# Optimization experiments

Measured on AMD Instinct MI355X. Metric: run time of the kernel, lower is better.

## Reference

```python
import jax, jax.numpy as jnp
import numpy as np
import math

B, S, HID = 2, 1024, 2048
N_HEAD, N_KV = 16, 4
HEAD = HID // N_HEAD          # 128
N_REP = N_HEAD // N_KV        # 4


def setup_inputs() -> dict:
    key = jax.random.key(0)
    ks = jax.random.split(key, 5)
    x = jax.random.normal(ks[0], (B, S, HID), dtype=jnp.float32)
    # realistic RoPE tables: freqs over half dim, duplicated (rotate_half convention)
    inv_freq = 1.0 / (10000.0 ** (np.arange(0, HEAD, 2, dtype=np.float32) / HEAD))
    t = np.arange(S, dtype=np.float32)
    freqs = np.outer(t, inv_freq)                    # [S, HEAD/2]
    emb = np.concatenate([freqs, freqs], axis=-1)    # [S, HEAD]
    cos = jnp.asarray(np.cos(emb), dtype=jnp.float32)
    sin = jnp.asarray(np.sin(emb), dtype=jnp.float32)
    sc = 0.02
    wq = jax.random.normal(ks[1], (HID, HID), dtype=jnp.float32) * sc
    wk = jax.random.normal(ks[2], (HID, N_KV * HEAD), dtype=jnp.float32) * sc
    wv = jax.random.normal(ks[3], (HID, N_KV * HEAD), dtype=jnp.float32) * sc
    wo = jax.random.normal(ks[4], (HID, HID), dtype=jnp.float32) * sc
    return {"x": x, "cos": cos, "sin": sin, "wq": wq, "wk": wk, "wv": wv, "wo": wo}


def _rotate_half(t):
    h = t.shape[-1] // 2
    return jnp.concatenate([-t[..., h:], t[..., :h]], axis=-1)


def reference(x, cos, sin, wq, wk, wv, wo):
    b, s, _ = x.shape
    q = (x @ wq).reshape(b, s, N_HEAD, HEAD)   # [B,S,H,D]
    k = (x @ wk).reshape(b, s, N_KV, HEAD)     # [B,S,Kv,D]
    v = (x @ wv).reshape(b, s, N_KV, HEAD)
    # RoPE: cos/sin [S,D] -> [S,1,D], broadcasts over batch and heads
    c = cos[:s, None, :]
    sn = sin[:s, None, :]
    q = q * c + _rotate_half(q) * sn
    k = k * c + _rotate_half(k) * sn
    # GQA: repeat kv heads to match query heads
    k = jnp.repeat(k, N_REP, axis=2)           # [B,S,H,D]
    v = jnp.repeat(v, N_REP, axis=2)
    q = q.transpose(0, 2, 1, 3)                # [B,H,S,D]
    k = k.transpose(0, 2, 1, 3)
    v = v.transpose(0, 2, 1, 3)
    scores = jnp.einsum("bhqd,bhkd->bhqk", q, k) / math.sqrt(HEAD)
    causal = jnp.triu(jnp.full((s, s), -jnp.inf, dtype=scores.dtype), k=1)
    scores = scores + causal[None, None, :, :]
    probs = jax.nn.softmax(scores.astype(jnp.float32), axis=-1).astype(q.dtype)
    out = jnp.einsum("bhqk,bhkd->bhqd", probs, v)   # [B,H,S,D]
    out = out.transpose(0, 2, 1, 3).reshape(b, s, N_HEAD * HEAD)
    return out @ wo
```

## Files before the change

### kernel.cpp

```cpp
#include <hip/hip_runtime.h>
#include <hip/hip_bf16.h>
#include <math.h>
#include <stdint.h>

#define BATCH 2
#define SEQ   1024
#define HID   2048
#define NH    16
#define NKV   4
#define HEAD  128
#define MROWS (BATCH*SEQ)
#define QSC   0.08838834764831845f

typedef _Float16 f16;
typedef _Float16 f16x8 __attribute__((ext_vector_type(8)));
typedef __fp16   h16x2 __attribute__((ext_vector_type(2)));
typedef float    f32x4 __attribute__((ext_vector_type(4)));

__device__ __forceinline__ void glds16(const void* g, void* l) {
    __builtin_amdgcn_global_load_lds(
        (const __attribute__((address_space(1))) void*)g,
        (__attribute__((address_space(3))) void*)l, 16, 0, 0);
}

__device__ __forceinline__ f32x4 mfma16(f16x8 a, f16x8 b, f32x4 c) {
    return __builtin_amdgcn_mfma_f32_16x16x32_f16(a, b, c, 0, 0, 0);
}

__global__ __launch_bounds__(256)
void prep(const float* __restrict__ x,
          const float* __restrict__ wq, const float* __restrict__ wk,
          const float* __restrict__ wv, const float* __restrict__ wo,
          f16* __restrict__ x16, f16* __restrict__ Wqkvt, f16* __restrict__ Wot)
{
    __shared__ float t[64][65];
    const int bid = blockIdx.x, tid = threadIdx.x;
    if (bid < 4096) {
        int i = bid * 256 + tid;
        float4 v = ((const float4*)x)[i];
        union { ushort4 u; f16 h[4]; } o;
        o.h[0] = (f16)v.x; o.h[1] = (f16)v.y; o.h[2] = (f16)v.z; o.h[3] = (f16)v.w;
        ((ushort4*)x16)[i] = o.u;
        return;
    }
    const float* W; int ld, cs, k0, n0; f16* out;
    if (bid < 5632) {
        int b2 = bid - 4096;
        n0 = (b2 % 48) * 64; k0 = (b2 / 48) * 64; out = Wqkvt;
        if (n0 < 2048)      { W = wq; ld = 2048; cs = n0; }
        else if (n0 < 2560) { W = wk; ld = 512;  cs = n0 - 2048; }
        else                { W = wv; ld = 512;  cs = n0 - 2560; }
    } else {
        int b3 = bid - 5632;
        n0 = (b3 % 32) * 64; k0 = (b3 / 32) * 64; out = Wot;
        W = wo; ld = 2048; cs = n0;
    }
    const int tr = tid >> 4, tc = tid & 15;
    #pragma unroll
    for (int i = 0; i < 4; ++i) {
        int row = tr * 4 + i;
        float4 v = *(const float4*)&W[(size_t)(k0 + row) * ld + cs + tc * 4];
        t[row][tc*4+0] = v.x; t[row][tc*4+1] = v.y;
        t[row][tc*4+2] = v.z; t[row][tc*4+3] = v.w;
    }
    __syncthreads();
    #pragma unroll
    for (int i = 0; i < 4; ++i) {
        int nrow = tr * 4 + i;
        union { ushort4 u; f16 h[4]; } o;
        o.h[0] = (f16)t[tc*4+0][nrow]; o.h[1] = (f16)t[tc*4+1][nrow];
        o.h[2] = (f16)t[tc*4+2][nrow]; o.h[3] = (f16)t[tc*4+3][nrow];
        *(ushort4*)&out[(size_t)(n0 + nrow) * 2048 + k0 + tc * 4] = o.u;
    }
}

template<int MODE>
__global__ __launch_bounds__(256)
void gemm16(const f16* __restrict__ A, const f16* __restrict__ Bt,
            f16* __restrict__ Oq, f16* __restrict__ Ok, f16* __restrict__ Ov,
            float* __restrict__ Of, int ntn)
{
    __shared__ f16 As[128 * 64];
    __shared__ f16 Bs[64 * 64];
    const int tid   = threadIdx.x;
    const int lane  = tid & 63;
    const int wid   = tid >> 6;
    const int col_l = lane & 15;
    const int hi    = lane >> 4;

    const int nwg = gridDim.x;
    const int cpx = nwg >> 3;
    const int bid = blockIdx.x;
    const int sw  = (bid & 7) * cpx + (bid >> 3);
    const int n0  = (sw % ntn) * 64;
    const int m0  = (sw / ntn) * 128;

    f32x4 acc[2][4];
    #pragma unroll
    for (int mt = 0; mt < 2; ++mt)
        #pragma unroll
        for (int nt = 0; nt < 4; ++nt)
            acc[mt][nt] = (f32x4){0.f, 0.f, 0.f, 0.f};

    #pragma unroll 1
    for (int kt = 0; kt < 32; ++kt) {
        #pragma unroll
        for (int j = 0; j < 4; ++j) {
            int gidx = j * 256 + tid;
            int r = gidx >> 3, g = gidx & 7;
            int gs = (g ^ (r & 7)) << 3;
            glds16(A + (size_t)(m0 + r) * 2048 + kt * 64 + gs,
                   (char*)As + (size_t)(j * 256 + (wid << 6)) * 16);
        }
        #pragma unroll
        for (int j = 0; j < 2; ++j) {
            int gidx = j * 256 + tid;
            int r = gidx >> 3, g = gidx & 7;
            int gs = (g ^ (r & 7)) << 3;
            glds16(Bt + (size_t)(n0 + r) * 2048 + kt * 64 + gs,
                   (char*)Bs + (size_t)(j * 256 + (wid << 6)) * 16);
        }
        asm volatile("s_waitcnt vmcnt(0)" ::: "memory");
        __syncthreads();

        #pragma unroll
        for (int ks = 0; ks < 2; ++ks) {
            int gr = (ks << 2) | hi;
            int ar0 = wid * 32 + col_l;
            int ar1 = ar0 + 16;
            f16x8 a0 = *(const f16x8*)&As[ar0 * 64 + ((gr ^ (ar0 & 7)) << 3)];
            f16x8 a1 = *(const f16x8*)&As[ar1 * 64 + ((gr ^ (ar1 & 7)) << 3)];
            #pragma unroll
            for (int nt = 0; nt < 4; ++nt) {
                int br = nt * 16 + col_l;
                f16x8 b = *(const f16x8*)&Bs[br * 64 + ((gr ^ (br & 7)) << 3)];
                acc[0][nt] = mfma16(a0, b, acc[0][nt]);
                acc[1][nt] = mfma16(a1, b, acc[1][nt]);
            }
        }
        __syncthreads();
    }

    if (MODE == 0) {
        #pragma unroll
        for (int mt = 0; mt < 2; ++mt)
            #pragma unroll
            for (int r = 0; r < 4; ++r) {
                int grow = m0 + wid * 32 + mt * 16 + hi * 4 + r;
                #pragma unroll
                for (int nt = 0; nt < 4; ++nt)
                    Of[(size_t)grow * 2048 + n0 + nt * 16 + col_l] = acc[mt][nt][r];
            }
    } else if (n0 < 2048) {
        #pragma unroll
        for (int mt = 0; mt < 2; ++mt)
            #pragma unroll
            for (int r = 0; r < 4; ++r) {
                int grow = m0 + wid * 32 + mt * 16 + hi * 4 + r;
                #pragma unroll
                for (int nt = 0; nt < 4; ++nt)
                    Oq[(size_t)grow * 2048 + n0 + nt * 16 + col_l] = (f16)acc[mt][nt][r];
            }
    } else if (n0 < 2560) {
        #pragma unroll
        for (int mt = 0; mt < 2; ++mt)
            #pragma unroll
            for (int r = 0; r < 4; ++r) {
                int grow = m0 + wid * 32 + mt * 16 + hi * 4 + r;
                #pragma unroll
                for (int nt = 0; nt < 4; ++nt)
                    Ok[(size_t)grow * 512 + (n0 - 2048) + nt * 16 + col_l] = (f16)acc[mt][nt][r];
            }
    } else {
        #pragma unroll
        for (int mt = 0; mt < 2; ++mt) {
            int grow0 = m0 + wid * 32 + mt * 16 + hi * 4;
            int bb = grow0 >> 10, s0 = grow0 & (SEQ - 1);
            #pragma unroll
            for (int nt = 0; nt < 4; ++nt) {
                int vcol = (n0 - 2560) + nt * 16 + col_l;
                int kvh = vcol >> 7, d = vcol & 127;
                union { ushort4 u; f16 h[4]; } pv;
                #pragma unroll
                for (int r = 0; r < 4; ++r) pv.h[r] = (f16)acc[mt][nt][r];
                *(ushort4*)&Ov[(size_t)((bb * 4 + kvh) * 128 + d) * 1024 + s0] = pv.u;
            }
        }
    }
}

__global__ __launch_bounds__(256)
void rope_k(f16* __restrict__ k16,
            const float* __restrict__ cosp, const float* __restrict__ sinp)
{
    int t = blockIdx.x * 256 + threadIdx.x;
    int row = t >> 6; int rem = t & 63; int head = rem >> 4; int quad = rem & 15;
    f16* p = k16 + (size_t)row * 512 + head * 128 + quad * 4;
    const int srow = row & (SEQ - 1);
    const int d0 = quad * 4;
    float4 c4 = *(const float4*)&cosp[srow * HEAD + d0];
    float4 s4 = *(const float4*)&sinp[srow * HEAD + d0];
    union { ushort4 u; f16 h[4]; } lo, hv, olo, ohi;
    lo.u = *(ushort4*)p;
    hv.u = *(ushort4*)(p + 64);
    const float c[4] = {c4.x, c4.y, c4.z, c4.w};
    const float s[4] = {s4.x, s4.y, s4.z, s4.w};
    #pragma unroll
    for (int e = 0; e < 4; ++e) {
        float fl = (float)lo.h[e], fh = (float)hv.h[e];
        olo.h[e] = (f16)(fl * c[e] - fh * s[e]);
        ohi.h[e] = (f16)(fh * c[e] + fl * s[e]);
    }
    *(ushort4*)p        = olo.u;
    *(ushort4*)(p + 64) = ohi.u;
}

__global__ __launch_bounds__(256, 2)
void attn16(const f16* __restrict__ q16, const f16* __restrict__ k16,
            const f16* __restrict__ vT,
            const float* __restrict__ cosp, const float* __restrict__ sinp,
            f16* __restrict__ attnb)
{
    __shared__ f16 Ks[2][64 * 128];
    __shared__ f16 Vs[2][128 * 64];

    const int tid   = threadIdx.x;
    const int lane  = tid & 63;
    const int wid   = tid >> 6;
    const int col_l = lane & 15;
    const int hi    = lane >> 4;

    const int bx = blockIdx.x;
    const int r8 = bx >> 8;
    const int c  = bx & 255;
    const int bh = c >> 3;
    const int j8 = c & 7;
    const int qt = r8 ? j8 : (15 - j8);
    const int b  = bh >> 4;
    const int h  = bh & 15;
    const int kv = h >> 2;
    const int qrow = qt * 64 + wid * 16 + col_l;

    f16x8 qf[4];
    {
        const f16* qp = q16 + (size_t)(b * SEQ + qrow) * 2048 + h * 128 + hi * 8;
        f16x8 raw[4];
        #pragma unroll
        for (int ks = 0; ks < 4; ++ks) raw[ks] = *(const f16x8*)&qp[ks * 32];
        #pragma unroll
        for (int ks = 0; ks < 2; ++ks) {
            union { float4 v; float a[4]; } c0, c1, s0, s1;
            const float* cp = cosp + qrow * HEAD + ks * 32 + hi * 8;
            const float* sp = sinp + qrow * HEAD + ks * 32 + hi * 8;
            c0.v = *(const float4*)cp;  c1.v = *(const float4*)(cp + 4);
            s0.v = *(const float4*)sp;  s1.v = *(const float4*)(sp + 4);
            #pragma unroll
            for (int e = 0; e < 8; ++e) {
                float cc = (e < 4) ? c0.a[e & 3] : c1.a[e & 3];
                float sv = (e < 4) ? s0.a[e & 3] : s1.a[e & 3];
                float lo = (float)raw[ks][e], hv = (float)raw[ks + 2][e];
                qf[ks][e]     = (f16)((lo * cc - hv * sv) * QSC);
                qf[ks + 2][e] = (f16)((hv * cc + lo * sv) * QSC);
            }
        }
    }
    const f16* vTg = vT + (size_t)(b * 4 + kv) * 128 * 1024;

    auto stage = [&](int buf, int kt) {
        #pragma unroll
        for (int j = 0; j < 4; ++j) {
            int gidx = j * 256 + tid;
            int r = gidx >> 4, g = gidx & 15;
            glds16(k16 + (size_t)(b * SEQ + kt * 64 + r) * 512 + kv * 128 + ((g ^ (r & 7)) << 3),
                   (char*)&Ks[buf][0] + (size_t)(j * 256 + (wid << 6)) * 16);
        }
        #pragma unroll
        for (int j = 0; j < 4; ++j) {
            int gidx = j * 256 + tid;
            int d = gidx >> 3, g = gidx & 7;
            glds16(vTg + (size_t)d * 1024 + kt * 64 + ((g ^ (d & 7)) << 3),
                   (char*)&Vs[buf][0] + (size_t)(j * 256 + (wid << 6)) * 16);
        }
    };

    f32x4 O[8];
    #pragma unroll
    for (int dt = 0; dt < 8; ++dt) O[dt] = (f32x4){0.f, 0.f, 0.f, 0.f};
    float mrun = -INFINITY, lrun = 0.f;

    const int ntiles = qt + 1;
    stage(0, 0);
    asm volatile("s_waitcnt vmcnt(0)" ::: "memory");
    __syncthreads();

    int cur = 0;
    #pragma unroll 1
    for (int kt = 0; kt < ntiles; ++kt) {
        if (kt + 1 < ntiles) stage(cur ^ 1, kt + 1);

        f32x4 S[4];
        #pragma unroll
        for (int t = 0; t < 4; ++t) S[t] = (f32x4){0.f, 0.f, 0.f, 0.f};
        #pragma unroll
        for (int ks = 0; ks < 4; ++ks) {
            int gr = (ks << 2) | hi;
            #pragma unroll
            for (int t = 0; t < 4; ++t) {
                int rr = t * 16 + col_l;
                f16x8 kf = *(const f16x8*)&Ks[cur][rr * 128 + ((gr ^ (rr & 7)) << 3)];
                S[t] = mfma16(kf, qf[ks], S[t]);
            }
        }
        float p[16];
        #pragma unroll
        for (int t = 0; t < 4; ++t) {
            p[t*4+0] = S[t][0]; p[t*4+1] = S[t][1];
            p[t*4+2] = S[t][2]; p[t*4+3] = S[t][3];
        }

        if (kt == qt) {
            #pragma unroll
            for (int sl = 0; sl < 16; ++sl) {
                int kk = kt * 64 + (sl >> 2) * 16 + hi * 4 + (sl & 3);
                if (kk > qrow) p[sl] = -INFINITY;
            }
        }

        float mt = p[0];
        #pragma unroll
        for (int sl = 1; sl < 16; ++sl) mt = fmaxf(mt, p[sl]);
        mt = fmaxf(mt, __shfl_xor(mt, 16));
        mt = fmaxf(mt, __shfl_xor(mt, 32));
        float mnew = fmaxf(mrun, mt);
        float corr = __expf(mrun - mnew);
        mrun = mnew;
        float ps = 0.f;
        #pragma unroll
        for (int sl = 0; sl < 16; ++sl) { p[sl] = __expf(p[sl] - mnew); ps += p[sl]; }
        ps += __shfl_xor(ps, 16);
        ps += __shfl_xor(ps, 32);
        lrun = lrun * corr + ps;

        union U2 { h16x2 h; int i; };
        int pk[8];
        #pragma unroll
        for (int t = 0; t < 4; ++t) {
            { U2 u; u.h = __builtin_amdgcn_cvt_pkrtz(p[t*4+0], p[t*4+1]); pk[t*2+0] = u.i; }
            { U2 u; u.h = __builtin_amdgcn_cvt_pkrtz(p[t*4+2], p[t*4+3]); pk[t*2+1] = u.i; }
        }
        union UA { f16x8 v; int i[4]; } F0, F1;
        #pragma unroll
        for (int j = 0; j < 4; ++j) {
            int srcl = col_l + 16 * ((2 * hi + (j >> 1)) & 3);
            int a0 = __builtin_amdgcn_ds_bpermute(srcl << 2, pk[j & 1]);
            int a1 = __builtin_amdgcn_ds_bpermute(srcl << 2, pk[2 + (j & 1)]);
            F0.i[j] = (hi >= 2) ? a1 : a0;
            int b0 = __builtin_amdgcn_ds_bpermute(srcl << 2, pk[4 + (j & 1)]);
            int b1 = __builtin_amdgcn_ds_bpermute(srcl << 2, pk[6 + (j & 1)]);
            F1.i[j] = (hi >= 2) ? b1 : b0;
        }

        float cb[4];
        #pragma unroll
        for (int r = 0; r < 4; ++r)
            cb[r] = __int_as_float(__builtin_amdgcn_ds_bpermute((hi * 4 + r) << 2,
                                                                __float_as_int(corr)));
        #pragma unroll
        for (int dt = 0; dt < 8; ++dt) {
            O[dt][0] *= cb[0]; O[dt][1] *= cb[1];
            O[dt][2] *= cb[2]; O[dt][3] *= cb[3];
        }

        #pragma unroll
        for (int dt = 0; dt < 8; ++dt) {
            int vr = dt * 16 + col_l;
            f16x8 v0 = *(const f16x8*)&Vs[cur][vr * 64 + ((hi ^ (vr & 7)) << 3)];
            O[dt] = mfma16(F0.v, v0, O[dt]);
            f16x8 v1 = *(const f16x8*)&Vs[cur][vr * 64 + (((4 | hi) ^ (vr & 7)) << 3)];
            O[dt] = mfma16(F1.v, v1, O[dt]);
        }

        if (kt + 1 < ntiles) {
            asm volatile("s_waitcnt vmcnt(0)" ::: "memory");
            __syncthreads();
            cur ^= 1;
        }
    }

    float linv = 1.f / lrun;
    float lb[4];
    #pragma unroll
    for (int r = 0; r < 4; ++r)
        lb[r] = __int_as_float(__builtin_amdgcn_ds_bpermute((hi * 4 + r) << 2,
                                                            __float_as_int(linv)));
    #pragma unroll
    for (int dt = 0; dt < 8; ++dt)
        #pragma unroll
        for (int r = 0; r < 4; ++r) {
            int row = b * SEQ + qt * 64 + wid * 16 + hi * 4 + r;
            attnb[(size_t)row * 2048 + h * 128 + dt * 16 + col_l] = (f16)(O[dt][r] * lb[r]);
        }
}

extern "C" void kernel_launch(void* const* d_in, const int* in_sizes, int n_in,
                              void* d_out, int out_size, void* d_ws, size_t ws_size,
                              hipStream_t stream)
{
    const float* x    = (const float*)d_in[0];
    const float* cosp = (const float*)d_in[1];
    const float* sinp = (const float*)d_in[2];
    const float* wq   = (const float*)d_in[3];
    const float* wk   = (const float*)d_in[4];
    const float* wv   = (const float*)d_in[5];
    const float* wo   = (const float*)d_in[6];
    float* out = (float*)d_out;

    char* ws = (char*)d_ws;
    f16* x16    = (f16*)(ws);
    f16* attn16v= (f16*)(ws);
    f16* Wqkvt  = (f16*)(ws + 8388608);
    f16* q16    = (f16*)(ws + 20971520);
    f16* k16    = (f16*)(ws + 29360128);
    f16* vT     = (f16*)(ws + 31457280);
    f16* Wot    = (f16*)(ws + 33554432);

    prep<<<6656, 256, 0, stream>>>(x, wq, wk, wv, wo, x16, Wqkvt, Wot);

    gemm16<1><<<768, 256, 0, stream>>>(x16, Wqkvt, q16, k16, vT, nullptr, 48);

    rope_k<<<512, 256, 0, stream>>>(k16, cosp, sinp);

    attn16<<<512, 256, 0, stream>>>(q16, k16, vT, cosp, sinp, attn16v);

    gemm16<0><<<512, 256, 0, stream>>>(attn16v, Wot, nullptr, nullptr, nullptr, out, 32);
}
```

Measured before the change: 203.9 us.

## Triple-buffer GEMM LDS tiles with K=32 steps and async prefetch

Replaces the single-buffered K=64 tile loop in the fp16 GEMM with a three-stage ring of K=32 LDS buffers. Global-to-LDS loads for tile kt+2 are issued while tile kt is computed, using partial vmcnt waits and one barrier per step instead of two. Adds an occupancy hint of 4 blocks per SM through launch_bounds. The trade is twice as many loop iterations with less MFMA work per barrier, a new swizzle pattern whose correctness depends on the vmcnt counting, and the risk that the register cap causes spills.

Result: slower. 210.0 us (+3.0%).

```diff
diff --git a/kernel.cpp b/kernel.cpp
--- a/kernel.cpp
+++ b/kernel.cpp
@@ -75,13 +75,13 @@
 }
 
 template<int MODE>
-__global__ __launch_bounds__(256)
+__global__ __launch_bounds__(256, 4)
 void gemm16(const f16* __restrict__ A, const f16* __restrict__ Bt,
             f16* __restrict__ Oq, f16* __restrict__ Ok, f16* __restrict__ Ov,
             float* __restrict__ Of, int ntn)
 {
-    __shared__ f16 As[128 * 64];
-    __shared__ f16 Bs[64 * 64];
+    __shared__ f16 As3[3][128 * 32];
+    __shared__ f16 Bs3[3][64 * 32];
     const int tid   = threadIdx.x;
     const int lane  = tid & 63;
     const int wid   = tid >> 6;
@@ -102,43 +102,54 @@
         for (int nt = 0; nt < 4; ++nt)
             acc[mt][nt] = (f32x4){0.f, 0.f, 0.f, 0.f};
 
-    #pragma unroll 1
-    for (int kt = 0; kt < 32; ++kt) {
-        #pragma unroll
-        for (int j = 0; j < 4; ++j) {
-            int gidx = j * 256 + tid;
-            int r = gidx >> 3, g = gidx & 7;
-            int gs = (g ^ (r & 7)) << 3;
-            glds16(A + (size_t)(m0 + r) * 2048 + kt * 64 + gs,
-                   (char*)As + (size_t)(j * 256 + (wid << 6)) * 16);
-        }
+    auto stage = [&](int buf, int kt) {
         #pragma unroll
         for (int j = 0; j < 2; ++j) {
             int gidx = j * 256 + tid;
-            int r = gidx >> 3, g = gidx & 7;
-            int gs = (g ^ (r & 7)) << 3;
-            glds16(Bt + (size_t)(n0 + r) * 2048 + kt * 64 + gs,
-                   (char*)Bs + (size_t)(j * 256 + (wid << 6)) * 16);
-        }
-        asm volatile("s_waitcnt vmcnt(0)" ::: "memory");
-        __syncthreads();
-
-        #pragma unroll
-        for (int ks = 0; ks < 2; ++ks) {
-            int gr = (ks << 2) | hi;
-            int ar0 = wid * 32 + col_l;
-            int ar1 = ar0 + 16;
-            f16x8 a0 = *(const f16x8*)&As[ar0 * 64 + ((gr ^ (ar0 & 7)) << 3)];
-            f16x8 a1 = *(const f16x8*)&As[ar1 * 64 + ((gr ^ (ar1 & 7)) << 3)];
-            #pragma unroll
-            for (int nt = 0; nt < 4; ++nt) {
-                int br = nt * 16 + col_l;
-                f16x8 b = *(const f16x8*)&Bs[br * 64 + ((gr ^ (br & 7)) << 3)];
-                acc[0][nt] = mfma16(a0, b, acc[0][nt]);
-                acc[1][nt] = mfma16(a1, b, acc[1][nt]);
-            }
-        }
-        __syncthreads();
+            int r = gidx >> 2, g = gidx & 3;
+            int gs = (g ^ ((r >> 1) & 3)) << 3;
+            glds16(A + (size_t)(m0 + r) * 2048 + kt * 32 + gs,
+                   (char*)&As3[buf][0] + (size_t)(j * 256 + (wid << 6)) * 16);
+        }
+        {
+            int r = tid >> 2, g = tid & 3;
+            int gs = (g ^ ((r >> 1) & 3)) << 3;
+            glds16(Bt + (size_t)(n0 + r) * 2048 + kt * 32 + gs,
+                   (char*)&Bs3[buf][0] + (size_t)(wid << 6) * 16);
+        }
+    };
+
+    stage(0, 0);
+    stage(1, 1);
+
+    const int ar0 = wid * 32 + col_l;
+    const int ar1 = ar0 + 16;
+    const int sg  = (hi ^ ((col_l >> 1) & 3)) << 3;
+
+    int cur = 0;
+    #pragma unroll 1
+    for (int kt = 0; kt < 64; ++kt) {
+        asm volatile("s_waitcnt lgkmcnt(0)" ::: "memory");
+        if (kt < 63) asm volatile("s_waitcnt vmcnt(3)" ::: "memory");
+        else         asm volatile("s_waitcnt vmcnt(0)" ::: "memory");
+        __builtin_amdgcn_s_barrier();
+        __builtin_amdgcn_sched_barrier(0);
+
+        f16x8 a0 = *(const f16x8*)&As3[cur][ar0 * 32 + sg];
+        f16x8 a1 = *(const f16x8*)&As3[cur][ar1 * 32 + sg];
+        #pragma unroll
+        for (int nt = 0; nt < 4; ++nt) {
+            int br = nt * 16 + col_l;
+            f16x8 b = *(const f16x8*)&Bs3[cur][br * 32 + sg];
+            acc[0][nt] = mfma16(a0, b, acc[0][nt]);
+            acc[1][nt] = mfma16(a1, b, acc[1][nt]);
+        }
+
+        if (kt + 2 < 64) {
+            int b2 = cur + 2; if (b2 >= 3) b2 -= 3;
+            stage(b2, kt + 2);
+        }
+        ++cur; if (cur == 3) cur = 0;
     }
 
     if (MODE == 0) {
```

## Double-buffer LDS tiles in gemm16 with two-deep async prefetch

Applied to the files above, without the earlier changes.

Adds a second LDS buffer for the A and B tiles in the projection GEMM and preloads two k-tiles. Each iteration waits only for the older stage with vmcnt(6), computes on it, then issues the load for tile kt+2 into the freed buffer. This overlaps global-to-LDS transfers with MFMA work instead of stalling on vmcnt(0) every iteration. The cost is twice the shared memory per block, which may reduce occupancy.

New measurement: 203.7 us. About the same (-0.1%).

```diff
diff --git a/kernel.cpp b/kernel.cpp
--- a/kernel.cpp
+++ b/kernel.cpp
@@ -80,8 +80,8 @@
             f16* __restrict__ Oq, f16* __restrict__ Ok, f16* __restrict__ Ov,
             float* __restrict__ Of, int ntn)
 {
-    __shared__ f16 As[128 * 64];
-    __shared__ f16 Bs[64 * 64];
+    __shared__ f16 As[2][128 * 64];
+    __shared__ f16 Bs[2][64 * 64];
     const int tid   = threadIdx.x;
     const int lane  = tid & 63;
     const int wid   = tid >> 6;
@@ -102,15 +102,14 @@
         for (int nt = 0; nt < 4; ++nt)
             acc[mt][nt] = (f32x4){0.f, 0.f, 0.f, 0.f};
 
-    #pragma unroll 1
-    for (int kt = 0; kt < 32; ++kt) {
+    auto stage = [&](int buf, int kt) {
         #pragma unroll
         for (int j = 0; j < 4; ++j) {
             int gidx = j * 256 + tid;
             int r = gidx >> 3, g = gidx & 7;
             int gs = (g ^ (r & 7)) << 3;
             glds16(A + (size_t)(m0 + r) * 2048 + kt * 64 + gs,
-                   (char*)As + (size_t)(j * 256 + (wid << 6)) * 16);
+                   (char*)&As[buf][0] + (size_t)(j * 256 + (wid << 6)) * 16);
         }
         #pragma unroll
         for (int j = 0; j < 2; ++j) {
@@ -118,27 +117,43 @@
             int r = gidx >> 3, g = gidx & 7;
             int gs = (g ^ (r & 7)) << 3;
             glds16(Bt + (size_t)(n0 + r) * 2048 + kt * 64 + gs,
-                   (char*)Bs + (size_t)(j * 256 + (wid << 6)) * 16);
-        }
-        asm volatile("s_waitcnt vmcnt(0)" ::: "memory");
-        __syncthreads();
+                   (char*)&Bs[buf][0] + (size_t)(j * 256 + (wid << 6)) * 16);
+        }
+    };
+
+    stage(0, 0);
+    stage(1, 1);
+
+    const int ar0 = wid * 32 + col_l;
+    const int ar1 = ar0 + 16;
+
+    int cur = 0;
+    #pragma unroll 1
+    for (int kt = 0; kt < 32; ++kt) {
+        if (kt < 31) asm volatile("s_waitcnt vmcnt(6)" ::: "memory");
+        else         asm volatile("s_waitcnt vmcnt(0)" ::: "memory");
+        __builtin_amdgcn_s_barrier();
+        __builtin_amdgcn_sched_barrier(0);
 
         #pragma unroll
         for (int ks = 0; ks < 2; ++ks) {
             int gr = (ks << 2) | hi;
-            int ar0 = wid * 32 + col_l;
-            int ar1 = ar0 + 16;
-            f16x8 a0 = *(const f16x8*)&As[ar0 * 64 + ((gr ^ (ar0 & 7)) << 3)];
-            f16x8 a1 = *(const f16x8*)&As[ar1 * 64 + ((gr ^ (ar1 & 7)) << 3)];
+            f16x8 a0 = *(const f16x8*)&As[cur][ar0 * 64 + ((gr ^ (ar0 & 7)) << 3)];
+            f16x8 a1 = *(const f16x8*)&As[cur][ar1 * 64 + ((gr ^ (ar1 & 7)) << 3)];
             #pragma unroll
             for (int nt = 0; nt < 4; ++nt) {
                 int br = nt * 16 + col_l;
-                f16x8 b = *(const f16x8*)&Bs[br * 64 + ((gr ^ (br & 7)) << 3)];
+                f16x8 b = *(const f16x8*)&Bs[cur][br * 64 + ((gr ^ (br & 7)) << 3)];
                 acc[0][nt] = mfma16(a0, b, acc[0][nt]);
                 acc[1][nt] = mfma16(a1, b, acc[1][nt]);
             }
         }
-        __syncthreads();
+
+        asm volatile("s_waitcnt lgkmcnt(0)" ::: "memory");
+        __builtin_amdgcn_sched_barrier(0);
+        __builtin_amdgcn_s_barrier();
+        if (kt + 2 < 32) stage(cur, kt + 2);
+        cur ^= 1;
     }
 
     if (MODE == 0) {
```
